# Performance work log

Hardware: AMD Instinct MI355X
Metric: run time of the kernel (lower is better)

The kernel has to match this reference:

```python
import jax, jax.numpy as jnp
import numpy as np
import math

D_MODEL = 1024
NUM_HEADS = 16
HEAD_DIM = D_MODEL // NUM_HEADS


def setup_inputs() -> dict:
    key = jax.random.key(0)
    ks = jax.random.split(key, 9)
    B, S = 2, 2048
    scale = 1.0 / math.sqrt(D_MODEL)
    x = jax.random.normal(ks[0], (B, S, D_MODEL), dtype=jnp.float32)
    # torch nn.Linear params: weight [out, in], bias [out]
    Wq = jax.random.normal(ks[1], (D_MODEL, D_MODEL), dtype=jnp.float32) * scale
    bq = jax.random.normal(ks[2], (D_MODEL,), dtype=jnp.float32) * scale
    Wk = jax.random.normal(ks[3], (D_MODEL, D_MODEL), dtype=jnp.float32) * scale
    bk = jax.random.normal(ks[4], (D_MODEL,), dtype=jnp.float32) * scale
    Wv = jax.random.normal(ks[5], (D_MODEL, D_MODEL), dtype=jnp.float32) * scale
    bv = jax.random.normal(ks[6], (D_MODEL,), dtype=jnp.float32) * scale
    Wo = jax.random.normal(ks[7], (D_MODEL, D_MODEL), dtype=jnp.float32) * scale
    bo = jax.random.normal(ks[8], (D_MODEL,), dtype=jnp.float32) * scale
    return {"x": x, "Wq": Wq, "bq": bq, "Wk": Wk, "bk": bk,
            "Wv": Wv, "bv": bv, "Wo": Wo, "bo": bo}


def reference(x, Wq, bq, Wk, bk, Wv, bv, Wo, bo):
    B, S, _ = x.shape
    H, Dh = NUM_HEADS, HEAD_DIM

    def proj(W, b):
        # torch Linear: x @ W.T + b -> [B,S,D] -> [B,H,S,Dh]
        y = jnp.einsum('bsd,ed->bse', x, W) + b
        return y.reshape(B, S, H, Dh).transpose(0, 2, 1, 3)

    Q = proj(Wq, bq)
    K = proj(Wk, bk)
    V = proj(Wv, bv)

    # scores [B,H,S,S], causal mask with -inf, then scale by 1/sqrt(head_dim)
    scores = jnp.einsum('bhqd,bhkd->bhqk', Q, K)
    causal = jnp.tril(jnp.ones((S, S), dtype=bool))
    scores = jnp.where(causal, scores, -jnp.inf)
    A = jax.nn.softmax(scores / math.sqrt(Dh), axis=-1)

    O = jnp.einsum('bhqk,bhkd->bhqd', A, V)  # [B,H,S,Dh]
    O = O.transpose(0, 2, 1, 3).reshape(B, S, H * Dh)
    return jnp.einsum('bsd,ed->bse', O, Wo) + bo
```

## Files before the change

kernel.cpp:

```cpp
#include <hip/hip_runtime.h>


typedef _Float16 f16x8 __attribute__((ext_vector_type(8)));
typedef _Float16 f16x4 __attribute__((ext_vector_type(4)));
typedef _Float16 f16x2 __attribute__((ext_vector_type(2)));
typedef float f32x4 __attribute__((ext_vector_type(4)));

#define S_  2048
#define DM  1024
#define NH  16
#define DH  64

__device__ __forceinline__ void gload_lds16(const void* g, void* s) {
  __builtin_amdgcn_global_load_lds(
      (const __attribute__((address_space(1))) void*)g,
      (__attribute__((address_space(3))) void*)s, 16, 0, 0);
}

__device__ __forceinline__ f16x2 pkrtz(float a, float b) {
  return __builtin_bit_cast(f16x2, __builtin_amdgcn_cvt_pkrtz(a, b));
}


__global__ void cvt_all_kernel(const float* __restrict__ x,
                               const float* __restrict__ w0,
                               const float* __restrict__ w1,
                               const float* __restrict__ w2,
                               const float* __restrict__ w3,
                               _Float16* __restrict__ xb,
                               _Float16* __restrict__ wb) {
  const int bid = blockIdx.x;
  const float* src;
  _Float16* dst;
  int idx;
  if (bid < 4096) {
    src = x; dst = xb; idx = bid * 256 + threadIdx.x;
  } else {
    const int j = bid - 4096;
    const int y = j >> 10;
    src = (y == 0) ? w0 : (y == 1) ? w1 : (y == 2) ? w2 : w3;
    dst = wb + (size_t)y * (DM * DM);
    idx = (j & 1023) * 256 + threadIdx.x;
  }
  const float4 v = ((const float4*)src)[idx];
  f16x4 h;
  h[0] = (_Float16)v.x; h[1] = (_Float16)v.y;
  h[2] = (_Float16)v.z; h[3] = (_Float16)v.w;
  ((f16x4*)dst)[idx] = h;
}


__global__ __launch_bounds__(256, 3) void gemm_qkv_kernel(
    const _Float16* __restrict__ xb, const _Float16* __restrict__ wb,
    const float* __restrict__ bq, const float* __restrict__ bk,
    const float* __restrict__ bv, _Float16* __restrict__ qkv)
{
  __shared__ _Float16 As[2][128 * 32];
  __shared__ _Float16 Ws[2][128 * 32];

  const int i = blockIdx.x;
  const int xcd = i & 7;
  const int tt = i >> 3;
  const int mp = xcd * 4 + (tt & 3);
  const int u = tt >> 2;
  const int np = u & 7;
  const int z = u >> 3;

  const _Float16* W = wb + (size_t)z * (DM * DM);
  const float* bias = (z == 0) ? bq : ((z == 1) ? bk : bv);
  _Float16* out = qkv + (size_t)z * 4194304;

  const f32x4 z4 = {0.f, 0.f, 0.f, 0.f};
  f32x4 acc[4][4];
#pragma unroll
  for (int mi = 0; mi < 4; ++mi)
#pragma unroll
    for (int ni = 0; ni < 4; ++ni) acc[mi][ni] = z4;

  const int m0 = mp * 128, n0 = np * 128;
  const int t = threadIdx.x;
  const int w = t >> 6, l = t & 63;
  const int quad = l >> 4, ln = l & 15;
  const int wm = (w >> 1) << 6, wn = (w & 1) << 6;
  const int srow = l >> 2, scol = (l & 3) << 3;

  for (int k0 = 0; k0 < DM; k0 += 64) {
#pragma unroll
    for (int h = 0; h < 2; ++h)
#pragma unroll
      for (int i2 = 0; i2 < 2; ++i2) {
        const int ra = w * 32 + i2 * 16;
        gload_lds16(&xb[(size_t)(m0 + ra + srow) * DM + k0 + h * 32 + scol],
                    &As[h][ra * 32]);
        gload_lds16(&W[(size_t)(n0 + ra + srow) * DM + k0 + h * 32 + scol],
                    &Ws[h][ra * 32]);
      }
    __syncthreads();

#pragma unroll
    for (int h = 0; h < 2; ++h) {
      f16x8 af[4], bf[4];
#pragma unroll
      for (int mi = 0; mi < 4; ++mi)
        af[mi] = *(const f16x8*)&As[h][(wm + mi * 16 + ln) * 32 + quad * 8];
#pragma unroll
      for (int ni = 0; ni < 4; ++ni)
        bf[ni] = *(const f16x8*)&Ws[h][(wn + ni * 16 + ln) * 32 + quad * 8];
#pragma unroll
      for (int mi = 0; mi < 4; ++mi)
#pragma unroll
        for (int ni = 0; ni < 4; ++ni)
          acc[mi][ni] = __builtin_amdgcn_mfma_f32_16x16x32_f16(
              af[mi], bf[ni], acc[mi][ni], 0, 0, 0);
    }
    __syncthreads();
  }

  const float scale = (z == 0) ? 0.18033688f : 1.0f;

#pragma unroll
  for (int ni = 0; ni < 4; ++ni) {
    const int c = n0 + wn + ni * 16 + ln;
    const float bias_c = bias[c];
    const int h = c >> 6, d = c & 63;
#pragma unroll
    for (int mi = 0; mi < 4; ++mi) {
      const int mb = m0 + wm + mi * 16 + quad * 4;
#pragma unroll
      for (int r = 0; r < 4; ++r) {
        const int mg = mb + r;
        const int b = mg >> 11, s = mg & 2047;
        const int bh = b * NH + h;
        const float v = (acc[mi][ni][r] + bias_c) * scale;
        size_t idx;
        if (z == 2)
          idx = (size_t)bh * 131072 + (s >> 5) * 2048 + (d >> 4) * 512 +
                ((s >> 3) & 3) * 128 + (d & 15) * 8 + (s & 7);
        else
          idx = (size_t)bh * 131072 + (s >> 4) * 1024 + (d >> 5) * 512 +
                ((d >> 3) & 3) * 128 + (s & 15) * 8 + (d & 7);
        out[idx] = (_Float16)v;
      }
    }
  }
}


__global__ __launch_bounds__(256, 2) void gemm_out_kernel(
    const _Float16* __restrict__ ob, const _Float16* __restrict__ wo,
    const float* __restrict__ bo, float* __restrict__ out)
{
  __shared__ _Float16 As[2][128 * 32];
  __shared__ _Float16 Ws[2][64 * 32];

  const int i = blockIdx.x;
  const int xcd = i & 7;
  const int tt = i >> 3;
  const int mp = xcd * 4 + (tt & 3);
  const int np = tt >> 2;

  const f32x4 z4 = {0.f, 0.f, 0.f, 0.f};
  f32x4 acc[2][4];
#pragma unroll
  for (int mi = 0; mi < 2; ++mi)
#pragma unroll
    for (int ni = 0; ni < 4; ++ni) acc[mi][ni] = z4;

  const int m0 = mp * 128, n0 = np * 64;
  const int t = threadIdx.x;
  const int w = t >> 6, l = t & 63;
  const int quad = l >> 4, ln = l & 15;
  const int srow = l >> 2, scol = (l & 3) << 3;

  for (int k0 = 0; k0 < DM; k0 += 64) {
#pragma unroll
    for (int h = 0; h < 2; ++h) {
#pragma unroll
      for (int i2 = 0; i2 < 2; ++i2) {
        const int ra = w * 32 + i2 * 16;
        gload_lds16(&ob[(size_t)(m0 + ra + srow) * DM + k0 + h * 32 + scol],
                    &As[h][ra * 32]);
      }
      gload_lds16(&wo[(size_t)(n0 + w * 16 + srow) * DM + k0 + h * 32 + scol],
                  &Ws[h][w * 16 * 32]);
    }
    __syncthreads();

#pragma unroll
    for (int h = 0; h < 2; ++h) {
      f16x8 af[2], bf[4];
#pragma unroll
      for (int mi = 0; mi < 2; ++mi)
        af[mi] = *(const f16x8*)&As[h][(w * 32 + mi * 16 + ln) * 32 + quad * 8];
#pragma unroll
      for (int ni = 0; ni < 4; ++ni)
        bf[ni] = *(const f16x8*)&Ws[h][(ni * 16 + ln) * 32 + quad * 8];
#pragma unroll
      for (int mi = 0; mi < 2; ++mi)
#pragma unroll
        for (int ni = 0; ni < 4; ++ni)
          acc[mi][ni] = __builtin_amdgcn_mfma_f32_16x16x32_f16(
              af[mi], bf[ni], acc[mi][ni], 0, 0, 0);
    }
    __syncthreads();
  }

#pragma unroll
  for (int ni = 0; ni < 4; ++ni) {
    const int c = n0 + ni * 16 + ln;
    const float bias_c = bo[c];
#pragma unroll
    for (int mi = 0; mi < 2; ++mi) {
      const int mb = m0 + w * 32 + mi * 16 + quad * 4;
#pragma unroll
      for (int r = 0; r < 4; ++r)
        out[(size_t)(mb + r) * DM + c] = acc[mi][ni][r] + bias_c;
    }
  }
}


template <int MODE>
__device__ __forceinline__ void tile64(
    const _Float16* __restrict__ kb_, const _Float16* __restrict__ vb_,
    int t, const f16x8 (&qf)[4][2], f32x4 (&oacc)[4][4], float (&l_i)[4],
    _Float16* Ps, int quad, int ln, int l)
{
  f16x8 kr[4], vr[4];
#pragma unroll
  for (int ii = 0; ii < 4; ++ii)
    kr[ii] = *(const f16x8*)(kb_ + (size_t)t * 2048 + ii * 512 + l * 8);
#pragma unroll
  for (int ii = 0; ii < 4; ++ii)
    vr[ii] = *(const f16x8*)(vb_ + (size_t)t * 2048 + ii * 512 + l * 8);

  const f32x4 z4 = {0.f, 0.f, 0.f, 0.f};
#pragma unroll
  for (int qs = 0; qs < 4; ++qs) {
    if (MODE == 2 && qs < 2) continue;

    f32x4 sacc[2];
    sacc[0] = z4; sacc[1] = z4;
#pragma unroll
    for (int ks = 0; ks < 2; ++ks)
#pragma unroll
      for (int mi = 0; mi < 2; ++mi)
        sacc[mi] = __builtin_amdgcn_mfma_f32_16x16x32_f16(
            kr[mi * 2 + ks], qf[qs][ks], sacc[mi], 0, 0, 0);

    const bool DG = (MODE == 1 && qs < 2) || (MODE == 2);
    const int hq = ((MODE == 1) ? qs : (qs - 2)) << 4;

    float rs = 0.f;
#pragma unroll
    for (int mi = 0; mi < 2; ++mi) {
      float p[4];
#pragma unroll
      for (int r = 0; r < 4; ++r) {
        p[r] = __builtin_amdgcn_exp2f(sacc[mi][r]);
        if (DG && (mi * 16 + quad * 4 + r > hq + ln)) p[r] = 0.f;
        rs += p[r];
      }
      const f16x2 lo = pkrtz(p[0], p[1]);
      const f16x2 hi = pkrtz(p[2], p[3]);
      const f16x4 pk = __builtin_shufflevector(lo, hi, 0, 1, 2, 3);
      const int slot = ((mi * 4 + quad) + 2 * ln) & 15;
      *(f16x4*)&Ps[ln * 64 + slot * 4] = pk;
    }
    l_i[qs] += rs;

    const int slot2 = ((quad * 2) + 2 * ln) & 15;
    const f16x8 pb = *(const f16x8*)&Ps[ln * 64 + slot2 * 4];

#pragma unroll
    for (int di = 0; di < 4; ++di)
      oacc[qs][di] = __builtin_amdgcn_mfma_f32_16x16x32_f16(
          vr[di], pb, oacc[qs][di], 0, 0, 0);
  }
}

__global__ __launch_bounds__(256, 3) void attn_kernel(
    const _Float16* __restrict__ QF, const _Float16* __restrict__ KF,
    const _Float16* __restrict__ VF, _Float16* __restrict__ Ob)
{
  __shared__ _Float16 Ps[4][1024];
  __shared__ float mrgO[2][4][1024];
  __shared__ float mrgL[2][4][64];

  const int i = blockIdx.x;
  const int bh = i & 31;
  const int qb = 31 - (i >> 5);

  const int tid = threadIdx.x;
  const int e = tid >> 6, l = tid & 63;
  const int quad = l >> 4, ln = l & 15;

  const _Float16* qb_ = QF + (size_t)bh * 131072;
  const _Float16* kb_ = KF + (size_t)bh * 131072;
  const _Float16* vb_ = VF + (size_t)bh * 131072;
  _Float16* psw = &Ps[e][0];
  const int bidx = bh >> 4, hh = bh & 15;

  f16x8 qf[4][2];
#pragma unroll
  for (int qs = 0; qs < 4; ++qs)
#pragma unroll
    for (int ks = 0; ks < 2; ++ks)
      qf[qs][ks] = *(const f16x8*)
          (qb_ + (size_t)((4 * qb + qs) * 2 + ks) * 512 + l * 8);

  const f32x4 z4 = {0.f, 0.f, 0.f, 0.f};
  f32x4 oacc[4][4];
#pragma unroll
  for (int qs = 0; qs < 4; ++qs)
#pragma unroll
    for (int di = 0; di < 4; ++di) oacc[qs][di] = z4;
  float l_i[4] = {0.f, 0.f, 0.f, 0.f};

  for (int t = e; t < 2 * qb; t += 4)
    tile64<0>(kb_, vb_, t, qf, oacc, l_i, psw, quad, ln, l);
  if (((2 * qb) & 3) == e)
    tile64<1>(kb_, vb_, 2 * qb, qf, oacc, l_i, psw, quad, ln, l);
  if (((2 * qb + 1) & 3) == e)
    tile64<2>(kb_, vb_, 2 * qb + 1, qf, oacc, l_i, psw, quad, ln, l);

  if (e & 1) {
    const int buf = e >> 1;
#pragma unroll
    for (int qs = 0; qs < 4; ++qs) {
#pragma unroll
      for (int di = 0; di < 4; ++di)
        *(f32x4*)&mrgO[buf][qs][di * 256 + l * 4] = oacc[qs][di];
      mrgL[buf][qs][l] = l_i[qs];
    }
  }
  __syncthreads();
  if (!(e & 1)) {
    const int buf = e >> 1;
#pragma unroll
    for (int qs = 0; qs < 4; ++qs) {
#pragma unroll
      for (int di = 0; di < 4; ++di)
        oacc[qs][di] += *(const f32x4*)&mrgO[buf][qs][di * 256 + l * 4];
      l_i[qs] += mrgL[buf][qs][l];
    }
  }
  __syncthreads();
  if (e == 2) {
#pragma unroll
    for (int qs = 0; qs < 4; ++qs) {
#pragma unroll
      for (int di = 0; di < 4; ++di)
        *(f32x4*)&mrgO[0][qs][di * 256 + l * 4] = oacc[qs][di];
      mrgL[0][qs][l] = l_i[qs];
    }
  }
  __syncthreads();
  if (e == 0) {
#pragma unroll
    for (int qs = 0; qs < 4; ++qs) {
#pragma unroll
      for (int di = 0; di < 4; ++di)
        oacc[qs][di] += *(const f32x4*)&mrgO[0][qs][di * 256 + l * 4];
      float li = l_i[qs] + mrgL[0][qs][l];
      li += __shfl_xor(li, 16);
      li += __shfl_xor(li, 32);
      const float inv = 1.0f / li;

      const int q = qb * 64 + qs * 16 + ln;
      _Float16* orow = Ob + (size_t)(bidx * S_ + q) * DM + hh * DH + quad * 4;
#pragma unroll
      for (int di = 0; di < 4; ++di) {
        f16x4 o4;
#pragma unroll
        for (int r = 0; r < 4; ++r)
          o4[r] = (_Float16)(oacc[qs][di][r] * inv);
        *(f16x4*)(orow + di * 16) = o4;
      }
    }
  }
}


extern "C" void kernel_launch(void* const* d_in, const int* in_sizes, int n_in,
                              void* d_out, int out_size, void* d_ws, size_t ws_size,
                              hipStream_t stream) {
  (void)in_sizes; (void)n_in; (void)out_size; (void)ws_size;
  const float* x  = (const float*)d_in[0];
  const float* Wq = (const float*)d_in[1];
  const float* bq = (const float*)d_in[2];
  const float* Wk = (const float*)d_in[3];
  const float* bk = (const float*)d_in[4];
  const float* Wv = (const float*)d_in[5];
  const float* bv = (const float*)d_in[6];
  const float* Wo = (const float*)d_in[7];
  const float* bo = (const float*)d_in[8];

  char* ws = (char*)d_ws;
  _Float16* xb  = (_Float16*)(ws);
  _Float16* wb  = (_Float16*)(ws + (8u << 20));
  _Float16* qkv = (_Float16*)(ws + (16u << 20));
  _Float16* ob  = (_Float16*)(ws + (40u << 20));

  cvt_all_kernel<<<dim3(8192), dim3(256), 0, stream>>>(x, Wq, Wk, Wv, Wo, xb, wb);
  gemm_qkv_kernel<<<dim3(768), dim3(256), 0, stream>>>(xb, wb, bq, bk, bv, qkv);
  attn_kernel<<<dim3(1024), dim3(256), 0, stream>>>(
      qkv, qkv + 4194304, qkv + 2 * 4194304, ob);
  gemm_out_kernel<<<dim3(512), dim3(256), 0, stream>>>(
      ob, wb + (size_t)3 * DM * DM, bo, (float*)d_out);
}
```

Measured before the change: 172.5 us.

## Software-pipeline K/V register loads in attention loop and relax occupancy bound

Splits the per-tile routine into a K/V load step and a compute step. The main loop now prefetches the next tile's K/V fragments into registers while computing the current one, so global load latency is hidden behind MFMA work. Launch bounds drop from 3 to 2 blocks per CU to make room for the extra registers. The cost is lower occupancy, which removes some of the latency hiding that came from running more waves.

```diff
diff --git a/kernel.cpp b/kernel.cpp
--- a/kernel.cpp
+++ b/kernel.cpp
@@ -220,20 +220,24 @@
 }
 
 
-template <int MODE>
-__device__ __forceinline__ void tile64(
+__device__ __forceinline__ void ldkv(
     const _Float16* __restrict__ kb_, const _Float16* __restrict__ vb_,
-    int t, const f16x8 (&qf)[4][2], f32x4 (&oacc)[4][4], float (&l_i)[4],
-    _Float16* Ps, int quad, int ln, int l)
+    int t, int l, f16x8 (&kr)[4], f16x8 (&vr)[4])
 {
-  f16x8 kr[4], vr[4];
 #pragma unroll
   for (int ii = 0; ii < 4; ++ii)
     kr[ii] = *(const f16x8*)(kb_ + (size_t)t * 2048 + ii * 512 + l * 8);
 #pragma unroll
   for (int ii = 0; ii < 4; ++ii)
     vr[ii] = *(const f16x8*)(vb_ + (size_t)t * 2048 + ii * 512 + l * 8);
-
+}
+
+template <int MODE>
+__device__ __forceinline__ void compute64(
+    const f16x8 (&kr)[4], const f16x8 (&vr)[4],
+    const f16x8 (&qf)[4][2], f32x4 (&oacc)[4][4], float (&l_i)[4],
+    _Float16* Ps, int quad, int ln)
+{
   const f32x4 z4 = {0.f, 0.f, 0.f, 0.f};
 #pragma unroll
   for (int qs = 0; qs < 4; ++qs) {
@@ -279,7 +283,7 @@
   }
 }
 
-__global__ __launch_bounds__(256, 3) void attn_kernel(
+__global__ __launch_bounds__(256, 2) void attn_kernel(
     const _Float16* __restrict__ QF, const _Float16* __restrict__ KF,
     const _Float16* __restrict__ VF, _Float16* __restrict__ Ob)
 {
@@ -317,12 +321,27 @@
     for (int di = 0; di < 4; ++di) oacc[qs][di] = z4;
   float l_i[4] = {0.f, 0.f, 0.f, 0.f};
 
-  for (int t = e; t < 2 * qb; t += 4)
-    tile64<0>(kb_, vb_, t, qf, oacc, l_i, psw, quad, ln, l);
-  if (((2 * qb) & 3) == e)
-    tile64<1>(kb_, vb_, 2 * qb, qf, oacc, l_i, psw, quad, ln, l);
-  if (((2 * qb + 1) & 3) == e)
-    tile64<2>(kb_, vb_, 2 * qb + 1, qf, oacc, l_i, psw, quad, ln, l);
+  f16x8 kr[4], vr[4];
+  int t = e;
+  if (t < 2 * qb) {
+    ldkv(kb_, vb_, t, l, kr, vr);
+    for (; t + 4 < 2 * qb; t += 4) {
+      f16x8 kn[4], vn[4];
+      ldkv(kb_, vb_, t + 4, l, kn, vn);
+      compute64<0>(kr, vr, qf, oacc, l_i, psw, quad, ln);
+#pragma unroll
+      for (int ii = 0; ii < 4; ++ii) { kr[ii] = kn[ii]; vr[ii] = vn[ii]; }
+    }
+    compute64<0>(kr, vr, qf, oacc, l_i, psw, quad, ln);
+  }
+  if (((2 * qb) & 3) == e) {
+    ldkv(kb_, vb_, 2 * qb, l, kr, vr);
+    compute64<1>(kr, vr, qf, oacc, l_i, psw, quad, ln);
+  }
+  if (((2 * qb + 1) & 3) == e) {
+    ldkv(kb_, vb_, 2 * qb + 1, l, kr, vr);
+    compute64<2>(kr, vr, qf, oacc, l_i, psw, quad, ln);
+  }
 
   if (e & 1) {
     const int buf = e >> 1;
```

Result: faster. 168.5 us (median of 2 runs) (-2.3%).
